# Performance work log

Hardware: AMD Instinct MI355X
Metric: run time of the kernel (lower is better)

## Reference

```python
import jax, jax.numpy as jnp
import numpy as np

B, S, D = 1, 2048, 2048
H, KVH, HD = 32, 8, 64  # heads, kv heads, head_dim
GROUPS = H // KVH
SCALE = HD ** -0.5


def rotate_half(x):
    x1, x2 = jnp.split(x, 2, axis=-1)
    return jnp.concatenate((-x2, x1), axis=-1)


def setup_inputs() -> dict:
    key = jax.random.key(0)
    ks = jax.random.split(key, 8)
    hidden_states = jax.random.normal(ks[0], (B, S, D), dtype=jnp.float32)
    # RoPE tables: [B, S, HD]
    inv_freq = 1.0 / (10000.0 ** (jnp.arange(0, HD, 2, dtype=jnp.float32) / HD))
    t = jnp.arange(S, dtype=jnp.float32)
    freqs = jnp.outer(t, inv_freq)                      # [S, HD/2]
    emb = jnp.concatenate((freqs, freqs), axis=-1)      # [S, HD]
    cos = jnp.cos(emb)[None]                            # [1, S, HD]
    sin = jnp.sin(emb)[None]
    std = 0.02
    wq = jax.random.normal(ks[1], (H * HD, D), dtype=jnp.float32) * std
    wk = jax.random.normal(ks[2], (KVH * HD, D), dtype=jnp.float32) * std
    wv = jax.random.normal(ks[3], (KVH * HD, D), dtype=jnp.float32) * std
    wo = jax.random.normal(ks[4], (D, H * HD), dtype=jnp.float32) * std
    return {"hidden_states": hidden_states, "cos": cos, "sin": sin,
            "wq": wq, "wk": wk, "wv": wv, "wo": wo}


def reference(hidden_states, cos, sin, wq, wk, wv, wo):
    b, s, d = hidden_states.shape
    # QKV projections (nn.Linear: x @ W.T), split into heads -> [B, H, S, HD]
    q = (hidden_states @ wq.T).reshape(b, s, H, HD).transpose(0, 2, 1, 3)
    k = (hidden_states @ wk.T).reshape(b, s, KVH, HD).transpose(0, 2, 1, 3)
    v = (hidden_states @ wv.T).reshape(b, s, KVH, HD).transpose(0, 2, 1, 3)
    # RoPE (unsqueeze_dim=1)
    c = cos[:, None, :, :]
    sn = sin[:, None, :, :]
    q = q * c + rotate_half(q) * sn
    k = k * c + rotate_half(k) * sn
    # GQA: repeat kv heads to match query heads
    k = jnp.repeat(k, GROUPS, axis=1)
    v = jnp.repeat(v, GROUPS, axis=1)
    # scaled causal softmax attention
    scores = jnp.einsum('bhqd,bhkd->bhqk', q, k) * SCALE
    causal = jnp.tril(jnp.ones((s, s), dtype=bool))
    scores = jnp.where(causal, scores, jnp.finfo(scores.dtype).min)
    probs = jax.nn.softmax(scores, axis=-1)
    attn = jnp.einsum('bhqk,bhkd->bhqd', probs, v)
    attn = attn.transpose(0, 2, 1, 3).reshape(b, s, H * HD)
    return attn @ wo.T
```

## Files before the change

### kernel.cpp

```cpp
#include <hip/hip_runtime.h>
#include <stdint.h>

#define SEQ   2048
#define DMODEL 2048
#define NQH   32
#define NKVH  8
#define HDIM  64
#define QN    (NQH*HDIM)
#define KVNN  (NKVH*HDIM)

typedef __bf16 bf16x8 __attribute__((ext_vector_type(8)));
typedef float  f32x4  __attribute__((ext_vector_type(4)));
typedef unsigned short u16;

__device__ __forceinline__ u16 f2bf(float f) {
  __bf16 h = (__bf16)f;
  return __builtin_bit_cast(u16, h);
}
__device__ __forceinline__ float bf2f(u16 b) {
  return __builtin_bit_cast(float, (uint32_t)b << 16);
}
__device__ __forceinline__ float fexp2(float x) {
#if __has_builtin(__builtin_amdgcn_exp2f)
  return __builtin_amdgcn_exp2f(x);
#else
  return __expf(0.69314718056f * x);
#endif
}
__device__ __forceinline__ bool probe_is_f32(const uint32_t* p) {
  return (p[0] & 0xFFFFu) == 0u;
}

__device__ __forceinline__ void glds16(const u16* g, void* lds) {
  __builtin_amdgcn_global_load_lds(
      (const __attribute__((address_space(1))) uint32_t*)g,
      (__attribute__((address_space(3))) uint32_t*)lds, 16, 0, 0);
}
__device__ __forceinline__ void wait_vm6() { asm volatile("s_waitcnt vmcnt(6)" ::: "memory"); }
__device__ __forceinline__ void wait_vm3() { asm volatile("s_waitcnt vmcnt(3)" ::: "memory"); }
__device__ __forceinline__ void wait_vm0() { asm volatile("s_waitcnt vmcnt(0)" ::: "memory"); }
__device__ __forceinline__ void raw_barrier() { __builtin_amdgcn_s_barrier(); }
__device__ __forceinline__ void mem_pin() { asm volatile("" ::: "memory"); }

__global__ __launch_bounds__(256)
void conv_all(const void* __restrict__ X, const void* __restrict__ cosv,
              const void* __restrict__ sinv, const void* __restrict__ wq,
              const void* __restrict__ wk, const void* __restrict__ wv,
              const void* __restrict__ wo,
              u16* __restrict__ Xc, u16* __restrict__ cosc, u16* __restrict__ sinc,
              u16* __restrict__ wqc, u16* __restrict__ wkc, u16* __restrict__ wvc,
              u16* __restrict__ woc)
{
  const bool f32in = probe_is_f32((const uint32_t*)cosv);
  const long t = (long)blockIdx.x * 256 + threadIdx.x;
  const void* src; u16* dst; long off;
  if      (t < 524288L)  { src = X;    dst = Xc;   off = t; }
  else if (t < 1048576L) { src = wq;   dst = wqc;  off = t - 524288L; }
  else if (t < 1179648L) { src = wk;   dst = wkc;  off = t - 1048576L; }
  else if (t < 1310720L) { src = wv;   dst = wvc;  off = t - 1179648L; }
  else if (t < 1835008L) { src = wo;   dst = woc;  off = t - 1310720L; }
  else if (t < 1851392L) { src = cosv; dst = cosc; off = t - 1835008L; }
  else                   { src = sinv; dst = sinc; off = t - 1851392L; }
  if (f32in) {
    const float4* s = (const float4*)src;
    float4 a = s[2*off], b = s[2*off + 1];
    union { u16 h[8]; uint4 u; } o;
    o.h[0]=f2bf(a.x); o.h[1]=f2bf(a.y); o.h[2]=f2bf(a.z); o.h[3]=f2bf(a.w);
    o.h[4]=f2bf(b.x); o.h[5]=f2bf(b.y); o.h[6]=f2bf(b.z); o.h[7]=f2bf(b.w);
    *(uint4*)(dst + off*8) = o.u;
  } else {
    *(uint4*)(dst + off*8) = ((const uint4*)src)[off];
  }
}

__global__ __launch_bounds__(256, 4)
void gemm_qkv(const u16* __restrict__ A,
              const u16* __restrict__ wq, const u16* __restrict__ wk,
              const u16* __restrict__ wv,
              u16* __restrict__ Qb, u16* __restrict__ Kb, u16* __restrict__ Vb)
{
  __shared__ __align__(16) u16 As[3][64][32];
  __shared__ __align__(16) u16 Bs[3][128][32];
  const int tid  = threadIdx.x;
  const int wave = tid >> 6;
  const int lane = tid & 63;
  const int quad = lane >> 4;
  const int l16  = lane & 15;
  const int m0 = blockIdx.y * 64;
  const int n0 = blockIdx.x * 128;
  const int wm = (wave & 1) * 32;
  const int wn = (wave >> 1) * 64;
  const int K = DMODEL;
  const int lr = lane >> 2;
  const int lc = (lane & 3) * 8;

  const u16* Bbase; u16* Cbase; int Cstride, nc0;
  if (n0 < 2048)      { Bbase = wq + (size_t)n0 * K;          Cbase = Qb; Cstride = QN;   nc0 = n0; }
  else if (n0 < 2560) { Bbase = wk + (size_t)(n0 - 2048) * K; Cbase = Kb; Cstride = KVNN; nc0 = n0 - 2048; }
  else                { Bbase = wv + (size_t)(n0 - 2560) * K; Cbase = Vb; Cstride = KVNN; nc0 = n0 - 2560; }

  f32x4 acc[2][4];
  #pragma unroll
  for (int i = 0; i < 2; i++)
    #pragma unroll
    for (int j = 0; j < 4; j++)
      acc[i][j] = (f32x4){0.f, 0.f, 0.f, 0.f};

  #define STAGE_QKV(b, k0)                                                        \
    do {                                                                          \
      glds16(A + (size_t)(m0 + 16*wave + lr) * K + (k0) + lc,                     \
             (char*)&As[b][0][0] + wave*1024);                                    \
      glds16(Bbase + (size_t)(16*wave + lr) * K + (k0) + lc,                      \
             (char*)&Bs[b][0][0] + wave*1024);                                    \
      glds16(Bbase + (size_t)(64 + 16*wave + lr) * K + (k0) + lc,                 \
             (char*)&Bs[b][0][0] + (4+wave)*1024);                                \
    } while (0)

  const int NT = K / 32;
  STAGE_QKV(0, 0);
  STAGE_QKV(1, 32);
  STAGE_QKV(2, 64);
  int cur = 0;
  for (int t = 0; t < NT; ++t) {
    if      (t < NT - 2) wait_vm6();
    else if (t == NT - 2) wait_vm3();
    else                  wait_vm0();
    raw_barrier();
    mem_pin();
    bf16x8 af[2], bfr[4];
    #pragma unroll
    for (int i = 0; i < 2; i++) af[i]  = *(const bf16x8*)&As[cur][wm + i*16 + l16][quad*8];
    #pragma unroll
    for (int j = 0; j < 4; j++) bfr[j] = *(const bf16x8*)&Bs[cur][wn + j*16 + l16][quad*8];
    #pragma unroll
    for (int i = 0; i < 2; i++)
      #pragma unroll
      for (int j = 0; j < 4; j++)
        acc[i][j] = __builtin_amdgcn_mfma_f32_16x16x32_bf16(af[i], bfr[j], acc[i][j], 0, 0, 0);
    raw_barrier();
    mem_pin();
    if (t + 3 < NT) STAGE_QKV(cur, (t + 3) * 32);
    cur = (cur == 2) ? 0 : cur + 1;
  }
  #undef STAGE_QKV

  #pragma unroll
  for (int i = 0; i < 2; i++) {
    const int rb = m0 + wm + i*16 + quad*4;
    #pragma unroll
    for (int j = 0; j < 4; j++) {
      const int col = nc0 + wn + j*16 + l16;
      #pragma unroll
      for (int r = 0; r < 4; r++)
        Cbase[(size_t)(rb + r) * Cstride + col] = f2bf(acc[i][j][r]);
    }
  }
}

__global__ __launch_bounds__(256, 4)
void gemm_nt(const u16* __restrict__ A, const u16* __restrict__ B,
             void* __restrict__ C, int M, int N, int K,
             const uint32_t* outprobe)
{
  __shared__ __align__(16) u16 As[3][64][32];
  __shared__ __align__(16) u16 Bs[3][128][32];
  const int tid  = threadIdx.x;
  const int wave = tid >> 6;
  const int lane = tid & 63;
  const int quad = lane >> 4;
  const int l16  = lane & 15;
  const int m0 = blockIdx.y * 64;
  const int n0 = blockIdx.x * 128;
  const int wm = (wave & 1) * 32;
  const int wn = (wave >> 1) * 64;
  const int lr = lane >> 2;
  const int lc = (lane & 3) * 8;

  f32x4 acc[2][4];
  #pragma unroll
  for (int i = 0; i < 2; i++)
    #pragma unroll
    for (int j = 0; j < 4; j++)
      acc[i][j] = (f32x4){0.f, 0.f, 0.f, 0.f};

  #define STAGE_NT(b, k0)                                                         \
    do {                                                                          \
      glds16(A + (size_t)(m0 + 16*wave + lr) * K + (k0) + lc,                     \
             (char*)&As[b][0][0] + wave*1024);                                    \
      glds16(B + (size_t)(n0 + 16*wave + lr) * K + (k0) + lc,                     \
             (char*)&Bs[b][0][0] + wave*1024);                                    \
      glds16(B + (size_t)(n0 + 64 + 16*wave + lr) * K + (k0) + lc,                \
             (char*)&Bs[b][0][0] + (4+wave)*1024);                                \
    } while (0)

  const int NT = K / 32;
  STAGE_NT(0, 0);
  STAGE_NT(1, 32);
  STAGE_NT(2, 64);
  int cur = 0;
  for (int t = 0; t < NT; ++t) {
    if      (t < NT - 2) wait_vm6();
    else if (t == NT - 2) wait_vm3();
    else                  wait_vm0();
    raw_barrier();
    mem_pin();
    bf16x8 af[2], bfr[4];
    #pragma unroll
    for (int i = 0; i < 2; i++) af[i]  = *(const bf16x8*)&As[cur][wm + i*16 + l16][quad*8];
    #pragma unroll
    for (int j = 0; j < 4; j++) bfr[j] = *(const bf16x8*)&Bs[cur][wn + j*16 + l16][quad*8];
    #pragma unroll
    for (int i = 0; i < 2; i++)
      #pragma unroll
      for (int j = 0; j < 4; j++)
        acc[i][j] = __builtin_amdgcn_mfma_f32_16x16x32_bf16(af[i], bfr[j], acc[i][j], 0, 0, 0);
    raw_barrier();
    mem_pin();
    if (t + 3 < NT) STAGE_NT(cur, (t + 3) * 32);
    cur = (cur == 2) ? 0 : cur + 1;
  }
  #undef STAGE_NT

  const bool f32out = (outprobe != nullptr) && probe_is_f32(outprobe);
  #pragma unroll
  for (int i = 0; i < 2; i++) {
    const int rb = m0 + wm + i*16 + quad*4;
    #pragma unroll
    for (int j = 0; j < 4; j++) {
      const int col = n0 + wn + j*16 + l16;
      if (f32out) {
        float* Cf = (float*)C;
        #pragma unroll
        for (int r = 0; r < 4; r++)
          Cf[(size_t)(rb + r) * N + col] = acc[i][j][r];
      } else {
        u16* Ch = (u16*)C;
        #pragma unroll
        for (int r = 0; r < 4; r++)
          Ch[(size_t)(rb + r) * N + col] = f2bf(acc[i][j][r]);
      }
    }
  }
}

__global__ void rope_k(u16* __restrict__ Kb,
                       const u16* __restrict__ cosb, const u16* __restrict__ sinb)
{
  const int idx = blockIdx.x * 256 + threadIdx.x;
  const int s = idx >> 8;
  const int rem = idx & 255;
  u16* base = Kb + (size_t)s * KVNN + (rem >> 5) * 64;
  const int d = rem & 31;
  const float x1 = bf2f(base[d]);
  const float x2 = bf2f(base[d + 32]);
  const float c  = bf2f(cosb[s * 64 + d]);
  const float sn = bf2f(sinb[s * 64 + d]);
  base[d]      = f2bf(x1 * c - x2 * sn);
  base[d + 32] = f2bf(x2 * c + x1 * sn);
}

__global__ __launch_bounds__(256)
void vtrans(const u16* __restrict__ Vb, u16* __restrict__ Vtg)
{
  __shared__ __align__(16) u16 T[64][72];
  const int tid = threadIdx.x;
  const int hkv = blockIdx.x & 7;
  const int s0  = (blockIdx.x >> 3) * 64;
  const int r = tid >> 3;
  const int c = (tid & 7) * 8;
  *(uint4*)&T[r][c]      = *(const uint4*)(Vb + (size_t)(s0 + r)      * KVNN + hkv*64 + c);
  *(uint4*)&T[r + 32][c] = *(const uint4*)(Vb + (size_t)(s0 + r + 32) * KVNN + hkv*64 + c);
  __syncthreads();
  #pragma unroll
  for (int dd = 0; dd < 64; dd += 32) {
    const int d = (tid >> 3) + dd;
    union { u16 h[8]; uint4 u; } o;
    #pragma unroll
    for (int j = 0; j < 8; j++) o.h[j] = T[c + j][d];
    *(uint4*)(Vtg + (size_t)(hkv*64 + d) * SEQ + s0 + c) = o.u;
  }
}

#define LOG2E 1.4426950408889634f

__device__ __forceinline__ float qmax16(float v) {
  v = fmaxf(v, __shfl_xor(v, 1)); v = fmaxf(v, __shfl_xor(v, 2));
  v = fmaxf(v, __shfl_xor(v, 4)); v = fmaxf(v, __shfl_xor(v, 8));
  return v;
}
__device__ __forceinline__ float qsum16(float v) {
  v += __shfl_xor(v, 1); v += __shfl_xor(v, 2);
  v += __shfl_xor(v, 4); v += __shfl_xor(v, 8);
  return v;
}

__global__ __launch_bounds__(256, 4)
void attn_kernel(const u16* __restrict__ Qb,
                 const u16* __restrict__ Kb,
                 const u16* __restrict__ Vtg,
                 u16* __restrict__ Ob,
                 const u16* __restrict__ cosb, const u16* __restrict__ sinb)
{
  __shared__ __align__(16) u16 Ks[64][72];
  __shared__ __align__(16) u16 Vt[64][72];
  __shared__ __align__(16) u16 Ps[4][16][72];

  const int tid  = threadIdx.x;
  const int wave = tid >> 6;
  const int lane = tid & 63;
  const int quad = lane >> 4;
  const int l16  = lane & 15;
  const int h    = blockIdx.x;
  const int qt   = 31 - blockIdx.y;
  const int hkv  = h >> 2;
  const int qrow0 = qt * 64 + wave * 16;
  const int ktmax = qt + 1;

  bf16x8 qf[2];
  {
    const int qrow = qrow0 + l16;
    const u16* qp = Qb + (size_t)qrow * QN + h*64 + quad*8;
    union { bf16x8 v; u16 h8[8]; } lo, hi, cv, sv, olo, ohi;
    lo.v = *(const bf16x8*)qp;
    hi.v = *(const bf16x8*)(qp + 32);
    cv.v = *(const bf16x8*)(cosb + qrow*64 + quad*8);
    sv.v = *(const bf16x8*)(sinb + qrow*64 + quad*8);
    #pragma unroll
    for (int j = 0; j < 8; j++) {
      const float x1 = bf2f(lo.h8[j]), x2 = bf2f(hi.h8[j]);
      const float c = bf2f(cv.h8[j]), sn = bf2f(sv.h8[j]);
      olo.h8[j] = f2bf((x1*c - x2*sn) * 0.125f);
      ohi.h8[j] = f2bf((x2*c + x1*sn) * 0.125f);
    }
    qf[0] = olo.v;
    qf[1] = ohi.v;
  }

  f32x4 oacc[4];
  #pragma unroll
  for (int nt = 0; nt < 4; nt++) oacc[nt] = (f32x4){0.f, 0.f, 0.f, 0.f};
  float m_run[4], l_run[4];
  #pragma unroll
  for (int r = 0; r < 4; r++) { m_run[r] = -1e30f; l_run[r] = 0.f; }

  const int sr = tid >> 3;
  const int sc = (tid & 7) * 8;

  uint4 k0, k1, v0, v1;
  {
    k0 = *(const uint4*)(Kb + (size_t)(sr)      * KVNN + hkv*64 + sc);
    k1 = *(const uint4*)(Kb + (size_t)(sr + 32) * KVNN + hkv*64 + sc);
    v0 = *(const uint4*)(Vtg + (size_t)(hkv*64 + sr)      * SEQ + sc);
    v1 = *(const uint4*)(Vtg + (size_t)(hkv*64 + sr + 32) * SEQ + sc);
  }

  for (int kt = 0; kt < ktmax; kt++) {
    const int kb = kt * 64;
    const bool diag = (kt == qt);

    __syncthreads();
    *(uint4*)&Ks[sr][sc]      = k0;
    *(uint4*)&Ks[sr + 32][sc] = k1;
    *(uint4*)&Vt[sr][sc]      = v0;
    *(uint4*)&Vt[sr + 32][sc] = v1;
    __syncthreads();

    if (kt + 1 < ktmax) {
      const int kn = kb + 64;
      k0 = *(const uint4*)(Kb + (size_t)(kn + sr)      * KVNN + hkv*64 + sc);
      k1 = *(const uint4*)(Kb + (size_t)(kn + sr + 32) * KVNN + hkv*64 + sc);
      v0 = *(const uint4*)(Vtg + (size_t)(hkv*64 + sr)      * SEQ + kn + sc);
      v1 = *(const uint4*)(Vtg + (size_t)(hkv*64 + sr + 32) * SEQ + kn + sc);
    }

    f32x4 sacc[4];
    #pragma unroll
    for (int nt = 0; nt < 4; nt++) sacc[nt] = (f32x4){0.f, 0.f, 0.f, 0.f};
    #pragma unroll
    for (int ks = 0; ks < 2; ks++)
      #pragma unroll
      for (int nt = 0; nt < 4; nt++)
        if (!diag || nt <= wave) {
          bf16x8 kf = *(const bf16x8*)&Ks[nt*16 + l16][ks*32 + quad*8];
          sacc[nt] = __builtin_amdgcn_mfma_f32_16x16x32_bf16(qf[ks], kf, sacc[nt], 0, 0, 0);
        }
    #pragma unroll
    for (int nt = 0; nt < 4; nt++)
      #pragma unroll
      for (int r = 0; r < 4; r++)
        sacc[nt][r] *= LOG2E;
    if (diag) {
      #pragma unroll
      for (int nt = 0; nt < 4; nt++)
        #pragma unroll
        for (int r = 0; r < 4; r++)
          if (kb + nt*16 + l16 > qrow0 + quad*4 + r)
            sacc[nt][r] = -1e30f;
    }
    float alpha[4];
    #pragma unroll
    for (int r = 0; r < 4; r++) {
      float mx = fmaxf(fmaxf(sacc[0][r], sacc[1][r]), fmaxf(sacc[2][r], sacc[3][r]));
      mx = qmax16(mx);
      const float mnew = fmaxf(m_run[r], mx);
      alpha[r] = fexp2(m_run[r] - mnew);
      m_run[r] = mnew;
      float rs = 0.f;
      #pragma unroll
      for (int nt = 0; nt < 4; nt++) {
        const float p = fexp2(sacc[nt][r] - mnew);
        rs += p;
        Ps[wave][quad*4 + r][nt*16 + l16] = f2bf(p);
      }
      rs = qsum16(rs);
      l_run[r] = l_run[r] * alpha[r] + rs;
    }
    #pragma unroll
    for (int nt = 0; nt < 4; nt++)
      #pragma unroll
      for (int r = 0; r < 4; r++)
        oacc[nt][r] *= alpha[r];
    asm volatile("" ::: "memory");
    #pragma unroll
    for (int ks = 0; ks < 2; ks++) {
      if (diag && wave < 2 && ks == 1) continue;
      bf16x8 pf = *(const bf16x8*)&Ps[wave][l16][ks*32 + quad*8];
      #pragma unroll
      for (int nt = 0; nt < 4; nt++) {
        bf16x8 vf = *(const bf16x8*)&Vt[nt*16 + l16][ks*32 + quad*8];
        oacc[nt] = __builtin_amdgcn_mfma_f32_16x16x32_bf16(pf, vf, oacc[nt], 0, 0, 0);
      }
    }
  }

  #pragma unroll
  for (int r = 0; r < 4; r++) {
    const float inv = 1.0f / l_run[r];
    const int qrow = qrow0 + quad*4 + r;
    #pragma unroll
    for (int nt = 0; nt < 4; nt++)
      Ob[(size_t)qrow * QN + h*64 + nt*16 + l16] = f2bf(oacc[nt][r] * inv);
  }
}

extern "C" void kernel_launch(void* const* d_in, const int* in_sizes, int n_in,
                              void* d_out, int out_size, void* d_ws, size_t ws_size,
                              hipStream_t stream) {
  const void* X    = d_in[0];
  const void* cosr = d_in[1];
  const void* sinr = d_in[2];
  const void* wq   = d_in[3];
  const void* wk   = d_in[4];
  const void* wv   = d_in[5];
  const void* wo   = d_in[6];

  char* ws = (char*)d_ws;
  const size_t MB = 1024u * 1024u;
  u16* Xc   = (u16*)(ws);
  u16* wqc  = (u16*)(ws + 8*MB);
  u16* wkc  = (u16*)(ws + 16*MB);
  u16* wvc  = (u16*)(ws + 18*MB);
  u16* woc  = (u16*)(ws + 20*MB);
  u16* cosc = (u16*)(ws + 28*MB);
  u16* sinc = (u16*)(ws + 28*MB + 256*1024);
  u16* Qb   = (u16*)(ws + 28*MB + 512*1024);
  u16* Kb   = (u16*)(ws + 36*MB + 512*1024);
  u16* Vb   = (u16*)(ws + 38*MB + 512*1024);
  u16* Vtg  = (u16*)(ws + 40*MB + 512*1024);
  u16* Ab   = wqc;

  dim3 blk(256);
  conv_all<<<dim3(7296), blk, 0, stream>>>(X, cosr, sinr, wq, wk, wv, wo,
                                           Xc, cosc, sinc, wqc, wkc, wvc, woc);
  gemm_qkv<<<dim3(24, 32), blk, 0, stream>>>(Xc, wqc, wkc, wvc, Qb, Kb, Vb);
  rope_k<<<dim3((SEQ*NKVH*32)/256), blk, 0, stream>>>(Kb, cosc, sinc);
  vtrans<<<dim3(256), blk, 0, stream>>>(Vb, Vtg);
  attn_kernel<<<dim3(NQH, SEQ/64), blk, 0, stream>>>(Qb, Kb, Vtg, Ab, cosc, sinc);
  gemm_nt<<<dim3(16, 32), blk, 0, stream>>>(Ab, woc, d_out, SEQ, DMODEL, DMODEL,
                                            (const uint32_t*)cosr);
}
```

Before: 249.9 us.

## Transpose attention MFMA operands so each lane owns one query row

Swaps the A/B operands of both attention MFMAs so the score and output accumulators are transposed: each lane now holds values for a single query row across 16 keys. Row max and row sum then take two cross-lane shuffles instead of four per row, and there is one running max/sum per lane instead of four. P is written to shared memory as packed 8-byte stores and the output as packed 8-byte global stores instead of scalar 2-byte stores. The aim is to cut shuffle, exp-bookkeeping and store instruction counts in the softmax inner loop.

```diff
diff --git a/kernel.cpp b/kernel.cpp
--- a/kernel.cpp
+++ b/kernel.cpp
@@ -283,17 +283,6 @@
 
 #define LOG2E 1.4426950408889634f
 
-__device__ __forceinline__ float qmax16(float v) {
-  v = fmaxf(v, __shfl_xor(v, 1)); v = fmaxf(v, __shfl_xor(v, 2));
-  v = fmaxf(v, __shfl_xor(v, 4)); v = fmaxf(v, __shfl_xor(v, 8));
-  return v;
-}
-__device__ __forceinline__ float qsum16(float v) {
-  v += __shfl_xor(v, 1); v += __shfl_xor(v, 2);
-  v += __shfl_xor(v, 4); v += __shfl_xor(v, 8);
-  return v;
-}
-
 __global__ __launch_bounds__(256, 4)
 void attn_kernel(const u16* __restrict__ Qb,
                  const u16* __restrict__ Kb,
@@ -315,6 +304,7 @@
   const int hkv  = h >> 2;
   const int qrow0 = qt * 64 + wave * 16;
   const int ktmax = qt + 1;
+  const int myq  = qrow0 + l16;
 
   bf16x8 qf[2];
   {
@@ -339,9 +329,7 @@
   f32x4 oacc[4];
   #pragma unroll
   for (int nt = 0; nt < 4; nt++) oacc[nt] = (f32x4){0.f, 0.f, 0.f, 0.f};
-  float m_run[4], l_run[4];
-  #pragma unroll
-  for (int r = 0; r < 4; r++) { m_run[r] = -1e30f; l_run[r] = 0.f; }
+  float m_run = -1e30f, l_run = 0.f;
 
   const int sr = tid >> 3;
   const int sc = (tid & 7) * 8;
@@ -382,7 +370,7 @@
       for (int nt = 0; nt < 4; nt++)
         if (!diag || nt <= wave) {
           bf16x8 kf = *(const bf16x8*)&Ks[nt*16 + l16][ks*32 + quad*8];
-          sacc[nt] = __builtin_amdgcn_mfma_f32_16x16x32_bf16(qf[ks], kf, sacc[nt], 0, 0, 0);
+          sacc[nt] = __builtin_amdgcn_mfma_f32_16x16x32_bf16(kf, qf[ks], sacc[nt], 0, 0, 0);
         }
     #pragma unroll
     for (int nt = 0; nt < 4; nt++)
@@ -394,32 +382,44 @@
       for (int nt = 0; nt < 4; nt++)
         #pragma unroll
         for (int r = 0; r < 4; r++)
-          if (kb + nt*16 + l16 > qrow0 + quad*4 + r)
+          if (kb + nt*16 + quad*4 + r > myq)
             sacc[nt][r] = -1e30f;
     }
-    float alpha[4];
-    #pragma unroll
-    for (int r = 0; r < 4; r++) {
-      float mx = fmaxf(fmaxf(sacc[0][r], sacc[1][r]), fmaxf(sacc[2][r], sacc[3][r]));
-      mx = qmax16(mx);
-      const float mnew = fmaxf(m_run[r], mx);
-      alpha[r] = fexp2(m_run[r] - mnew);
-      m_run[r] = mnew;
-      float rs = 0.f;
-      #pragma unroll
-      for (int nt = 0; nt < 4; nt++) {
+    float mx = sacc[0][0];
+    #pragma unroll
+    for (int nt = 0; nt < 4; nt++)
+      #pragma unroll
+      for (int r = 0; r < 4; r++)
+        if (nt | r) mx = fmaxf(mx, sacc[nt][r]);
+    mx = fmaxf(mx, __shfl_xor(mx, 16));
+    mx = fmaxf(mx, __shfl_xor(mx, 32));
+    const float mnew = fmaxf(m_run, mx);
+    const float alpha = fexp2(m_run - mnew);
+    m_run = mnew;
+    float rs = 0.f;
+    #pragma unroll
+    for (int nt = 0; nt < 4; nt++)
+      #pragma unroll
+      for (int r = 0; r < 4; r++) {
         const float p = fexp2(sacc[nt][r] - mnew);
+        sacc[nt][r] = p;
         rs += p;
-        Ps[wave][quad*4 + r][nt*16 + l16] = f2bf(p);
       }
-      rs = qsum16(rs);
-      l_run[r] = l_run[r] * alpha[r] + rs;
+    rs += __shfl_xor(rs, 16);
+    rs += __shfl_xor(rs, 32);
+    l_run = l_run * alpha + rs;
+    #pragma unroll
+    for (int nt = 0; nt < 4; nt++) {
+      union { u16 h[4]; uint2 v; } pk;
+      #pragma unroll
+      for (int r = 0; r < 4; r++) pk.h[r] = f2bf(sacc[nt][r]);
+      *(uint2*)&Ps[wave][l16][nt*16 + quad*4] = pk.v;
     }
     #pragma unroll
     for (int nt = 0; nt < 4; nt++)
       #pragma unroll
       for (int r = 0; r < 4; r++)
-        oacc[nt][r] *= alpha[r];
+        oacc[nt][r] *= alpha;
     asm volatile("" ::: "memory");
     #pragma unroll
     for (int ks = 0; ks < 2; ks++) {
@@ -428,18 +428,20 @@
       #pragma unroll
       for (int nt = 0; nt < 4; nt++) {
         bf16x8 vf = *(const bf16x8*)&Vt[nt*16 + l16][ks*32 + quad*8];
-        oacc[nt] = __builtin_amdgcn_mfma_f32_16x16x32_bf16(pf, vf, oacc[nt], 0, 0, 0);
+        oacc[nt] = __builtin_amdgcn_mfma_f32_16x16x32_bf16(vf, pf, oacc[nt], 0, 0, 0);
       }
     }
   }
 
-  #pragma unroll
-  for (int r = 0; r < 4; r++) {
-    const float inv = 1.0f / l_run[r];
-    const int qrow = qrow0 + quad*4 + r;
-    #pragma unroll
-    for (int nt = 0; nt < 4; nt++)
-      Ob[(size_t)qrow * QN + h*64 + nt*16 + l16] = f2bf(oacc[nt][r] * inv);
+  {
+    const float inv = 1.0f / l_run;
+    #pragma unroll
+    for (int nt = 0; nt < 4; nt++) {
+      union { u16 h[4]; uint2 v; } ok;
+      #pragma unroll
+      for (int r = 0; r < 4; r++) ok.h[r] = f2bf(oacc[nt][r] * inv);
+      *(uint2*)(Ob + (size_t)myq * QN + h*64 + nt*16 + quad*4) = ok.v;
+    }
   }
 }
 
```

New measurement: 227.0 us. 9.2% less time.
